# Kernel optimization log

Hardware: AMD Instinct MI355X
Metric: run time of the kernel (lower is better)

Reference implementation:

```python
import jax, jax.numpy as jnp
import numpy as np

D_MODEL = 1024
NUM_HEADS = 16
HEAD_DIM = D_MODEL // NUM_HEADS
LN_EPS = 1e-3  # Keras LayerNormalization default epsilon


def setup_inputs() -> dict:
    key = jax.random.key(0)
    ks = jax.random.split(key, 7)
    s = 1.0 / np.sqrt(D_MODEL)
    return {
        "x": jax.random.normal(ks[0], (2, 2048, D_MODEL), dtype=jnp.float32),
        "Wq": jax.random.normal(ks[1], (D_MODEL, D_MODEL), dtype=jnp.float32) * s,
        "bq": jnp.zeros((D_MODEL,), dtype=jnp.float32),
        "Wk": jax.random.normal(ks[2], (D_MODEL, D_MODEL), dtype=jnp.float32) * s,
        "bk": jnp.zeros((D_MODEL,), dtype=jnp.float32),
        "Wv": jax.random.normal(ks[3], (D_MODEL, D_MODEL), dtype=jnp.float32) * s,
        "bv": jnp.zeros((D_MODEL,), dtype=jnp.float32),
        "ln_gamma": jnp.ones((D_MODEL,), dtype=jnp.float32),
        "ln_beta": jnp.zeros((D_MODEL,), dtype=jnp.float32),
    }


def _split_heads(t):
    # [B, S, D] -> [B, H, S, Dh]; matches tf.split(axis=2)+concat(axis=0) math
    B, S, D = t.shape
    return t.reshape(B, S, NUM_HEADS, HEAD_DIM).transpose(0, 2, 1, 3)


def reference(x, Wq, bq, Wk, bk, Wv, bv, ln_gamma, ln_beta):
    Q = _split_heads(x @ Wq + bq)   # [B,H,S,Dh]
    K = _split_heads(x @ Wk + bk)
    V = _split_heads(x @ Wv + bv)
    scale = 1.0 / jnp.sqrt(jnp.asarray(HEAD_DIM, dtype=x.dtype))
    scores = jnp.einsum("bhqd,bhkd->bhqk", Q, K) * scale
    probs = jax.nn.softmax(scores, axis=-1)  # dropout is identity at inference
    ctx = jnp.einsum("bhqk,bhkd->bhqd", probs, V)
    out = ctx.transpose(0, 2, 1, 3).reshape(x.shape)  # merge heads -> [B,S,D]
    out = out + x  # residual
    mean = jnp.mean(out, axis=-1, keepdims=True)
    var = jnp.mean(jnp.square(out - mean), axis=-1, keepdims=True)
    return (out - mean) * jax.lax.rsqrt(var + LN_EPS) * ln_gamma + ln_beta
```

## Files before the change

kernel.cpp:

```cpp
#include <hip/hip_runtime.h>
#include <stdint.h>

#define D_MODEL 1024
#define SEQ     2048
#define BATCH   2
#define NHEADS  16
#define HDIM    64
#define ROWS    (BATCH*SEQ)

typedef __attribute__((ext_vector_type(8)))  short short8;
typedef __attribute__((ext_vector_type(4)))  float f32x4;
typedef __attribute__((ext_vector_type(16))) float f32x16;
typedef __attribute__((ext_vector_type(4)))  short short4v;

__device__ __forceinline__ unsigned short f2bf(float f){
  union { float f; unsigned int u; } v; v.f = f;
  unsigned int r = v.u + 0x7fffu + ((v.u >> 16) & 1u);
  return (unsigned short)(r >> 16);
}

__device__ __forceinline__ float fast_exp2(float x){
  float r;
  asm("v_exp_f32 %0, %1" : "=v"(r) : "v"(x));
  return r;
}

__device__ __forceinline__ float f3(float a, float b, float c){
  return fmaxf(fmaxf(a,b),c);
}

__device__ __forceinline__ void gload16(const void* g, void* l){
  __builtin_amdgcn_global_load_lds((__attribute__((address_space(1))) void*)(uintptr_t)g,
                                   (__attribute__((address_space(3))) void*)l, 16, 0, 0);
}

__global__ __launch_bounds__(256) void prep(const float* __restrict__ x,
                                            const float* __restrict__ Wq,
                                            const float* __restrict__ Wk,
                                            const float* __restrict__ Wv,
                                            unsigned short* __restrict__ xb,
                                            unsigned short* __restrict__ Wt){
  __shared__ float tile[32][33];
  const int bidx = blockIdx.x;
  if (bidx < 4096){
    const int i = bidx*256 + threadIdx.x;
    float4 v = ((const float4*)x)[i];
    short4v o;
    o[0] = (short)f2bf(v.x); o[1] = (short)f2bf(v.y);
    o[2] = (short)f2bf(v.z); o[3] = (short)f2bf(v.w);
    ((short4v*)xb)[i] = o;
  } else {
    const int wz  = bidx - 4096;
    const int mat = wz >> 10;
    const int idx = wz & 1023;
    const float* W = (mat==0)?Wq:((mat==1)?Wk:Wv);
    unsigned short* dst = Wt + (size_t)mat*1048576;
    const int tx = threadIdx.x & 31, ty = threadIdx.x >> 5;
    const int n0 = (idx & 31)*32, k0 = (idx >> 5)*32;
    #pragma unroll
    for (int j=0;j<32;j+=8)
      tile[ty+j][tx] = W[(size_t)(k0+ty+j)*D_MODEL + n0+tx];
    __syncthreads();
    #pragma unroll
    for (int j=0;j<32;j+=8)
      dst[(size_t)(n0+ty+j)*D_MODEL + k0+tx] = f2bf(tile[tx][ty+j]);
  }
}

__global__ __launch_bounds__(256) void qkv_gemm(
    const unsigned short* __restrict__ xb, const unsigned short* __restrict__ wtb,
    const float* __restrict__ bq, const float* __restrict__ bk, const float* __restrict__ bv,
    unsigned short* __restrict__ qb, unsigned short* __restrict__ kbuf,
    unsigned short* __restrict__ vtb)
{
  __shared__ unsigned short As[128*32];
  __shared__ unsigned short Bs[128*32];
  const int mat = blockIdx.z;
  const unsigned short* wt = wtb + (size_t)mat*1048576;
  const float* bias = (mat==0)?bq:((mat==1)?bk:bv);
  const float osc = (mat==0)?0.18033688011112042f:1.0f;
  const int bm = blockIdx.x, bn = blockIdx.y;
  const int t = threadIdx.x, w = t>>6, lane = t&63;
  const int g = lane>>4, l15 = lane&15;
  const int wm = w>>1, wn = w&1;

  const int srow = (w<<5) + (lane>>2);
  const int scol = (lane&3)*8;

  f32x4 acc[4][4];
  #pragma unroll
  for (int i=0;i<4;++i)
    #pragma unroll
    for (int j=0;j<4;++j) acc[i][j] = (f32x4){0.f,0.f,0.f,0.f};

  for (int kt=0; kt<32; ++kt){
    const int k0 = kt*32;
    #pragma unroll
    for (int j=0;j<2;++j){
      gload16(xb + (size_t)(bm*128 + srow + j*16)*D_MODEL + k0 + scol, &As[(w<<10)+(j<<9)]);
      gload16(wt + (size_t)(bn*128 + srow + j*16)*D_MODEL + k0 + scol, &Bs[(w<<10)+(j<<9)]);
    }
    __syncthreads();
    short8 a[4], b[4];
    #pragma unroll
    for (int mr=0;mr<4;++mr) a[mr] = *(const short8*)&As[(wm*64 + mr*16 + l15)*32 + g*8];
    #pragma unroll
    for (int nr=0;nr<4;++nr) b[nr] = *(const short8*)&Bs[(wn*64 + nr*16 + l15)*32 + g*8];
    #pragma unroll
    for (int mr=0;mr<4;++mr)
      #pragma unroll
      for (int nr=0;nr<4;++nr)
        acc[mr][nr] = __builtin_amdgcn_mfma_f32_16x16x32_bf16(a[mr], b[nr], acc[mr][nr], 0,0,0);
    __syncthreads();
  }
  #pragma unroll
  for (int mr=0;mr<4;++mr){
    const int rowb = bm*128 + wm*64 + mr*16 + g*4;
    #pragma unroll
    for (int nr=0;nr<4;++nr){
      const int col = bn*128 + wn*64 + nr*16 + l15;
      const float bsv = bias[col];
      const int h = col>>6, d = col&63;
      #pragma unroll
      for (int r=0;r<4;++r){
        const int m = rowb + r;
        const int b_ = m>>11, s = m&2047;
        const unsigned short val = f2bf((acc[mr][nr][r] + bsv)*osc);
        if (mat==2)
          vtb [(((size_t)(b_*NHEADS + h))*HDIM + d)*SEQ + s] = val;
        else if (mat==0)
          qb  [(((size_t)(b_*NHEADS + h))*SEQ + s)*HDIM + d] = val;
        else
          kbuf[(((size_t)(b_*NHEADS + h))*SEQ + s)*HDIM + d] = val;
      }
    }
  }
}

__global__ __launch_bounds__(256, 2) void attn_fwd(
  const unsigned short* __restrict__ Qb, const unsigned short* __restrict__ Kb,
  const unsigned short* __restrict__ Vtb, float* __restrict__ ctx)
{
  __shared__ unsigned short Ks[2][4096];
  __shared__ unsigned short Vs[2][4096];
  const int lin = blockIdx.x;
  const int bh = (lin&7)*4 + (lin>>7);
  const int q0 = ((lin>>3)&15)*128;
  const int t = threadIdx.x, w = t>>6, lane = t&63;
  const int l31 = lane&31, hi = lane>>5;
  const unsigned short* Qh  = Qb  + (size_t)bh*SEQ*HDIM;
  const unsigned short* Kh  = Kb  + (size_t)bh*SEQ*HDIM;
  const unsigned short* Vth = Vtb + (size_t)bh*HDIM*SEQ;

  const int qrow = q0 + w*32 + l31;
  short8 qf[4];
  #pragma unroll
  for (int dht=0;dht<4;++dht)
    qf[dht] = *(const short8*)&Qh[(size_t)qrow*HDIM + dht*16 + hi*8];

  const int srow0 = t>>3,        srow1 = (256+t)>>3;
  const int skk0  = ((t&7)<<3) ^ ((srow0&7)<<3);
  const int skk1  = ((t&7)<<3) ^ ((srow1&7)<<3);
  const int rx    = l31&7;

  float m = 0.f;
  float rsum = 0.f;
  f32x16 o0, o1;
  #pragma unroll
  for (int r=0;r<16;++r){ o0[r]=0.f; o1[r]=0.f; }

#define STAGE(buf, ktile) do {                                                    \
    const int kb_ = (ktile)*64;                                                   \
    gload16(&Kh[(size_t)(kb_ + srow0)*HDIM + skk0], &Ks[buf][(w*64)*8]);          \
    gload16(&Kh[(size_t)(kb_ + srow1)*HDIM + skk1], &Ks[buf][(256 + w*64)*8]);    \
    gload16(&Vth[(size_t)srow0*SEQ + kb_ + skk0],   &Vs[buf][(w*64)*8]);          \
    gload16(&Vth[(size_t)srow1*SEQ + kb_ + skk1],   &Vs[buf][(256 + w*64)*8]);    \
  } while(0)

#define BODY(CUR, KT, FIRST) do {                                                 \
    if ((KT) < 31) STAGE((CUR)^1, (KT)+1);                                        \
                                       \
    f32x16 s0, s1;                                                                \
    _Pragma("unroll")                                                             \
    for (int r=0;r<16;++r){ s0[r]=0.f; s1[r]=0.f; }                               \
    __builtin_amdgcn_s_setprio(1);                                                \
    _Pragma("unroll")                                                             \
    for (int dht=0;dht<4;++dht){                                                  \
      short8 kf = *(const short8*)&Ks[CUR][l31*64 + (((dht<<1)|hi) ^ rx)*8];      \
      s0 = __builtin_amdgcn_mfma_f32_32x32x16_bf16(kf, qf[dht], s0, 0,0,0);       \
    }                                                                             \
    _Pragma("unroll")                                                             \
    for (int dht=0;dht<4;++dht){                                                  \
      short8 kf = *(const short8*)&Ks[CUR][(32+l31)*64 + (((dht<<1)|hi) ^ rx)*8]; \
      s1 = __builtin_amdgcn_mfma_f32_32x32x16_bf16(kf, qf[dht], s1, 0,0,0);       \
    }                                                                             \
    __builtin_amdgcn_s_setprio(0);                                                \
    if (FIRST){                                                                   \
      float a0=f3(s0[0],s0[1],s0[2]),  a1=f3(s0[3],s0[4],s0[5]);                  \
      float a2=f3(s0[6],s0[7],s0[8]),  a3=f3(s0[9],s0[10],s0[11]);                \
      float a4=f3(s0[12],s0[13],s0[14]), a5=f3(s0[15],s1[0],s1[1]);               \
      float a6=f3(s1[2],s1[3],s1[4]),  a7=f3(s1[5],s1[6],s1[7]);                  \
      float a8=f3(s1[8],s1[9],s1[10]), a9=f3(s1[11],s1[12],s1[13]);               \
      float a10=fmaxf(s1[14],s1[15]);                                             \
      float rmx = f3(f3(a0,a1,a2), f3(a3,a4,a5), f3(f3(a6,a7,a8), a9, a10));      \
      m = fmaxf(rmx, __shfl_xor(rmx, 32));                                        \
    }                                                                             \
          \
    unsigned int u[8], vv[8];                                                     \
    _Pragma("unroll")                                                             \
    for (int i=0;i<8;++i){                                                        \
      float e0 = fast_exp2(s0[2*i]   - m);                                        \
      float e1 = fast_exp2(s0[2*i+1] - m);                                        \
      float e2 = fast_exp2(s1[2*i]   - m);                                        \
      float e3 = fast_exp2(s1[2*i+1] - m);                                        \
      rsum += (e0+e1)+(e2+e3);                                                    \
      asm("v_cvt_pk_bf16_f32 %0, %1, %2" : "=v"(u[i])  : "v"(e0), "v"(e1));       \
      asm("v_cvt_pk_bf16_f32 %0, %1, %2" : "=v"(vv[i]) : "v"(e2), "v"(e3));       \
    }                                                                             \
    asm("v_permlane32_swap_b32 %0, %1" : "+v"(u[0]),  "+v"(u[2]));                \
    asm("v_permlane32_swap_b32 %0, %1" : "+v"(u[1]),  "+v"(u[3]));                \
    asm("v_permlane32_swap_b32 %0, %1" : "+v"(u[4]),  "+v"(u[6]));                \
    asm("v_permlane32_swap_b32 %0, %1" : "+v"(u[5]),  "+v"(u[7]));                \
    asm("v_permlane32_swap_b32 %0, %1" : "+v"(vv[0]), "+v"(vv[2]));               \
    asm("v_permlane32_swap_b32 %0, %1" : "+v"(vv[1]), "+v"(vv[3]));               \
    asm("v_permlane32_swap_b32 %0, %1" : "+v"(vv[4]), "+v"(vv[6]));               \
    asm("v_permlane32_swap_b32 %0, %1" : "+v"(vv[5]), "+v"(vv[7]));               \
    union U8 { unsigned int wq[4]; short8 s; };                                   \
    short8 pa[4];                                                                 \
    { U8 x; x.wq[0]=u[0];  x.wq[1]=u[1];  x.wq[2]=u[2];  x.wq[3]=u[3];  pa[0]=x.s; } \
    { U8 x; x.wq[0]=u[4];  x.wq[1]=u[5];  x.wq[2]=u[6];  x.wq[3]=u[7];  pa[1]=x.s; } \
    { U8 x; x.wq[0]=vv[0]; x.wq[1]=vv[1]; x.wq[2]=vv[2]; x.wq[3]=vv[3]; pa[2]=x.s; } \
    { U8 x; x.wq[0]=vv[4]; x.wq[1]=vv[5]; x.wq[2]=vv[6]; x.wq[3]=vv[7]; pa[3]=x.s; } \
                                                                    \
    __builtin_amdgcn_s_setprio(1);                                                \
    _Pragma("unroll")                                                             \
    for (int kb=0;kb<4;++kb){                                                     \
      short8 vf0 = *(const short8*)&Vs[CUR][l31*64      + (((kb<<1)|hi) ^ rx)*8]; \
      short8 vf1 = *(const short8*)&Vs[CUR][(32+l31)*64 + (((kb<<1)|hi) ^ rx)*8]; \
      o0 = __builtin_amdgcn_mfma_f32_32x32x16_bf16(pa[kb], vf0, o0, 0,0,0);       \
      o1 = __builtin_amdgcn_mfma_f32_32x32x16_bf16(pa[kb], vf1, o1, 0,0,0);       \
    }                                                                             \
    __builtin_amdgcn_s_setprio(0);                                                \
    if ((KT) < 31) __syncthreads();                                               \
  } while(0)

  STAGE(0, 0);
  __syncthreads();

  BODY(0, 0, 1);
  BODY(1, 1, 0);
  for (int kt2=2; kt2<32; kt2+=2){
    BODY(0, kt2,   0);
    BODY(1, kt2+1, 0);
  }
#undef BODY
#undef STAGE

  const float rst = rsum + __shfl_xor(rsum, 32);
  const int b_ = bh>>4, h = bh&15;
  #pragma unroll
  for (int r=0;r<16;++r){
    const int cr = (r&3) + ((r>>2)<<3) + (hi<<2);
    const float inv = 1.0f / __shfl(rst, cr);
    const int s = q0 + w*32 + cr;
    float* dst = &ctx[((size_t)(b_*SEQ + s))*D_MODEL + h*64];
    dst[l31]      = o0[r] * inv;
    dst[32 + l31] = o1[r] * inv;
  }
}

__global__ __launch_bounds__(256) void resid_ln(
  const float* __restrict__ ctx, const float* __restrict__ x,
  const float* __restrict__ gamma, const float* __restrict__ beta,
  float* __restrict__ out)
{
  const int row = blockIdx.x, t = threadIdx.x;
  const size_t base = (size_t)row*D_MODEL;
  float4 c  = ((const float4*)(ctx + base))[t];
  float4 xr = ((const float4*)(x   + base))[t];
  float4 v; v.x=c.x+xr.x; v.y=c.y+xr.y; v.z=c.z+xr.z; v.w=c.w+xr.w;
  float s  = v.x+v.y+v.z+v.w;
  float ss = v.x*v.x+v.y*v.y+v.z*v.z+v.w*v.w;
  #pragma unroll
  for (int m=1;m<64;m<<=1){ s += __shfl_xor(s,m); ss += __shfl_xor(ss,m); }
  __shared__ float red[8];
  const int w = t>>6;
  if ((t&63)==0){ red[w] = s; red[4+w] = ss; }
  __syncthreads();
  s  = red[0]+red[1]+red[2]+red[3];
  ss = red[4]+red[5]+red[6]+red[7];
  const float mean = s*(1.f/D_MODEL);
  const float var  = ss*(1.f/D_MODEL) - mean*mean;
  const float rstd = rsqrtf(var + 1e-3f);
  float4 gv = ((const float4*)gamma)[t], bv = ((const float4*)beta)[t];
  float4 ov;
  ov.x=(v.x-mean)*rstd*gv.x+bv.x; ov.y=(v.y-mean)*rstd*gv.y+bv.y;
  ov.z=(v.z-mean)*rstd*gv.z+bv.z; ov.w=(v.w-mean)*rstd*gv.w+bv.w;
  ((float4*)(out + base))[t] = ov;
}

extern "C" void kernel_launch(void* const* d_in, const int* in_sizes, int n_in,
                              void* d_out, int out_size, void* d_ws, size_t ws_size,
                              hipStream_t stream){
  const float* x     = (const float*)d_in[0];
  const float* Wq    = (const float*)d_in[1];
  const float* bq    = (const float*)d_in[2];
  const float* Wk    = (const float*)d_in[3];
  const float* bk    = (const float*)d_in[4];
  const float* Wv    = (const float*)d_in[5];
  const float* bv    = (const float*)d_in[6];
  const float* gamma = (const float*)d_in[7];
  const float* beta  = (const float*)d_in[8];
  float* out = (float*)d_out;

  char* ws = (char*)d_ws;
  unsigned short* xb  = (unsigned short*)(ws);
  unsigned short* wtb = (unsigned short*)(ws + 8388608);
  unsigned short* qb  = (unsigned short*)(ws + 14680064);
  unsigned short* kb  = (unsigned short*)(ws + 23068672);
  unsigned short* vtb = (unsigned short*)(ws + 31457280);
  float* ctx          = (float*)(ws + 39845888);

  hipLaunchKernelGGL(prep,     dim3(7168),              dim3(256), 0, stream,
                     x, Wq, Wk, Wv, xb, wtb);
  hipLaunchKernelGGL(qkv_gemm, dim3(32,8,3),            dim3(256), 0, stream,
                     xb, wtb, bq, bk, bv, qb, kb, vtb);
  hipLaunchKernelGGL(attn_fwd, dim3(512),               dim3(256), 0, stream, qb, kb, vtb, ctx);
  hipLaunchKernelGGL(resid_ln, dim3(ROWS),              dim3(256), 0, stream, ctx, x, gamma, beta, out);
}
```

Measured before the change: 109.5 us.

## Stage V transpose through LDS and store attention context as bf16

The V projection epilogue now writes its tile into a padded LDS buffer, then emits coalesced 16-byte stores along the sequence dimension. This replaces scattered 2-byte strided writes to the transposed V layout. Separately, the attention output context is stored as bf16 instead of fp32, which halves its write and its later read in the residual+LayerNorm kernel. The cost is extra LDS (about 34KB) in the GEMM kernel, which may reduce occupancy, and a precision loss on the context before the residual add.

```diff
diff --git a/kernel.cpp b/kernel.cpp
--- a/kernel.cpp
+++ b/kernel.cpp
@@ -17,6 +17,12 @@
   union { float f; unsigned int u; } v; v.f = f;
   unsigned int r = v.u + 0x7fffu + ((v.u >> 16) & 1u);
   return (unsigned short)(r >> 16);
+}
+
+__device__ __forceinline__ float bf2f(short u){
+  union { unsigned int i; float f; } w;
+  w.i = ((unsigned int)(unsigned short)u) << 16;
+  return w.f;
 }
 
 __device__ __forceinline__ float fast_exp2(float x){
@@ -75,6 +81,7 @@
 {
   __shared__ unsigned short As[128*32];
   __shared__ unsigned short Bs[128*32];
+  __shared__ unsigned short vt_lds[128*136];
   const int mat = blockIdx.z;
   const unsigned short* wt = wtb + (size_t)mat*1048576;
   const float* bias = (mat==0)?bq:((mat==1)?bk:bv);
@@ -113,33 +120,54 @@
         acc[mr][nr] = __builtin_amdgcn_mfma_f32_16x16x32_bf16(a[mr], b[nr], acc[mr][nr], 0,0,0);
     __syncthreads();
   }
-  #pragma unroll
-  for (int mr=0;mr<4;++mr){
-    const int rowb = bm*128 + wm*64 + mr*16 + g*4;
-    #pragma unroll
-    for (int nr=0;nr<4;++nr){
-      const int col = bn*128 + wn*64 + nr*16 + l15;
-      const float bsv = bias[col];
-      const int h = col>>6, d = col&63;
+
+  if (mat != 2){
+    unsigned short* outp = (mat==0)?qb:kbuf;
+    #pragma unroll
+    for (int mr=0;mr<4;++mr){
+      const int rowb = bm*128 + wm*64 + mr*16 + g*4;
       #pragma unroll
-      for (int r=0;r<4;++r){
-        const int m = rowb + r;
-        const int b_ = m>>11, s = m&2047;
-        const unsigned short val = f2bf((acc[mr][nr][r] + bsv)*osc);
-        if (mat==2)
-          vtb [(((size_t)(b_*NHEADS + h))*HDIM + d)*SEQ + s] = val;
-        else if (mat==0)
-          qb  [(((size_t)(b_*NHEADS + h))*SEQ + s)*HDIM + d] = val;
-        else
-          kbuf[(((size_t)(b_*NHEADS + h))*SEQ + s)*HDIM + d] = val;
+      for (int nr=0;nr<4;++nr){
+        const int col = bn*128 + wn*64 + nr*16 + l15;
+        const float bsv = bias[col];
+        const int h = col>>6, d = col&63;
+        #pragma unroll
+        for (int r=0;r<4;++r){
+          const int m = rowb + r;
+          const int b_ = m>>11, s = m&2047;
+          outp[(((size_t)(b_*NHEADS + h))*SEQ + s)*HDIM + d] = f2bf((acc[mr][nr][r] + bsv)*osc);
+        }
       }
     }
+  } else {
+    #pragma unroll
+    for (int mr=0;mr<4;++mr){
+      const int rowb = wm*64 + mr*16 + g*4;
+      #pragma unroll
+      for (int nr=0;nr<4;++nr){
+        const int col = wn*64 + nr*16 + l15;
+        const float bsv = bias[bn*128 + col];
+        #pragma unroll
+        for (int r=0;r<4;++r)
+          vt_lds[col*136 + rowb + r] = f2bf(acc[mr][nr][r] + bsv);
+      }
+    }
+    __syncthreads();
+    const int c  = t>>1;
+    const int sh = (t&1)*64;
+    const int h  = bn*2 + (c>>6), d = c&63;
+    const int b_ = (bm*128)>>11;
+    const int s0 = (bm*128)&2047;
+    unsigned short* dst = vtb + (((size_t)(b_*NHEADS + h))*HDIM + d)*SEQ + s0 + sh;
+    #pragma unroll
+    for (int j=0;j<8;++j)
+      *(short8*)(dst + j*8) = *(const short8*)&vt_lds[c*136 + sh + j*8];
   }
 }
 
 __global__ __launch_bounds__(256, 2) void attn_fwd(
   const unsigned short* __restrict__ Qb, const unsigned short* __restrict__ Kb,
-  const unsigned short* __restrict__ Vtb, float* __restrict__ ctx)
+  const unsigned short* __restrict__ Vtb, unsigned short* __restrict__ ctxb)
 {
   __shared__ unsigned short Ks[2][4096];
   __shared__ unsigned short Vs[2][4096];
@@ -263,22 +291,26 @@
     const int cr = (r&3) + ((r>>2)<<3) + (hi<<2);
     const float inv = 1.0f / __shfl(rst, cr);
     const int s = q0 + w*32 + cr;
-    float* dst = &ctx[((size_t)(b_*SEQ + s))*D_MODEL + h*64];
-    dst[l31]      = o0[r] * inv;
-    dst[32 + l31] = o1[r] * inv;
+    unsigned short* dst = ctxb + ((size_t)(b_*SEQ + s))*D_MODEL + h*64;
+    dst[l31]      = f2bf(o0[r] * inv);
+    dst[32 + l31] = f2bf(o1[r] * inv);
   }
 }
 
 __global__ __launch_bounds__(256) void resid_ln(
-  const float* __restrict__ ctx, const float* __restrict__ x,
+  const unsigned short* __restrict__ ctxb, const float* __restrict__ x,
   const float* __restrict__ gamma, const float* __restrict__ beta,
   float* __restrict__ out)
 {
   const int row = blockIdx.x, t = threadIdx.x;
   const size_t base = (size_t)row*D_MODEL;
-  float4 c  = ((const float4*)(ctx + base))[t];
-  float4 xr = ((const float4*)(x   + base))[t];
-  float4 v; v.x=c.x+xr.x; v.y=c.y+xr.y; v.z=c.z+xr.z; v.w=c.w+xr.w;
+  short4v c4 = ((const short4v*)(ctxb + base))[t];
+  float4 xr  = ((const float4*)(x + base))[t];
+  float4 v;
+  v.x = bf2f(c4[0]) + xr.x;
+  v.y = bf2f(c4[1]) + xr.y;
+  v.z = bf2f(c4[2]) + xr.z;
+  v.w = bf2f(c4[3]) + xr.w;
   float s  = v.x+v.y+v.z+v.w;
   float ss = v.x*v.x+v.y*v.y+v.z*v.z+v.w*v.w;
   #pragma unroll
@@ -319,12 +351,12 @@
   unsigned short* qb  = (unsigned short*)(ws + 14680064);
   unsigned short* kb  = (unsigned short*)(ws + 23068672);
   unsigned short* vtb = (unsigned short*)(ws + 31457280);
-  float* ctx          = (float*)(ws + 39845888);
+  unsigned short* ctxb= (unsigned short*)(ws + 39845888);
 
   hipLaunchKernelGGL(prep,     dim3(7168),              dim3(256), 0, stream,
                      x, Wq, Wk, Wv, xb, wtb);
   hipLaunchKernelGGL(qkv_gemm, dim3(32,8,3),            dim3(256), 0, stream,
                      xb, wtb, bq, bk, bv, qb, kb, vtb);
-  hipLaunchKernelGGL(attn_fwd, dim3(512),               dim3(256), 0, stream, qb, kb, vtb, ctx);
-  hipLaunchKernelGGL(resid_ln, dim3(ROWS),              dim3(256), 0, stream, ctx, x, gamma, beta, out);
-}
+  hipLaunchKernelGGL(attn_fwd, dim3(512),               dim3(256), 0, stream, qb, kb, vtb, ctxb);
+  hipLaunchKernelGGL(resid_ln, dim3(ROWS),              dim3(256), 0, stream, ctxb, x, gamma, beta, out);
+}
```

New measurement: 114.9 us. 1.05x slower.
